# Performance work log

Hardware: AMD Instinct MI355X
Metric: run time of the kernel (lower is better)

Reference implementation:

```python
import jax, jax.numpy as jnp
import numpy as np

N = 10000      # nodes
E = 80000      # edges
D = 128        # d_model
H = 8          # num_heads
DH = 128       # d_head
DFF = 512      # d_ff
CLAMP = 5.0
EPS = 1e-5


def setup_inputs() -> dict:
    key = jax.random.key(0)
    ks = jax.random.split(key, 10)
    s = 0.05
    return {
        "feat": jax.random.normal(ks[0], (N, D), jnp.float32),
        "src": jax.random.randint(ks[1], (E,), 0, N),
        "dst": jax.random.randint(ks[2], (E,), 0, N),
        # projections stored as (in, out); x @ W == torch Linear(bias=False)
        "Wq": jax.random.normal(ks[3], (D, H * DH), jnp.float32) * s,
        "Wk": jax.random.normal(ks[4], (D, H * DH), jnp.float32) * s,
        "Wv": jax.random.normal(ks[5], (D, H * DH), jnp.float32) * s,
        "Wo": jax.random.normal(ks[6], (H * DH, D), jnp.float32) * s,
        "g1": jnp.ones((D,), jnp.float32),
        "b1": jnp.zeros((D,), jnp.float32),
        "W1": jax.random.normal(ks[7], (D, DFF), jnp.float32) * s,
        "bf1": jnp.zeros((DFF,), jnp.float32),
        "W2": jax.random.normal(ks[8], (DFF, D), jnp.float32) * s,
        "bf2": jnp.zeros((D,), jnp.float32),
        "g2": jnp.ones((D,), jnp.float32),
        "b2": jnp.zeros((D,), jnp.float32),
    }


def _layer_norm(x, g, b):
    mu = x.mean(-1, keepdims=True)
    xc = x - mu
    var = (xc * xc).mean(-1, keepdims=True)
    return xc * jax.lax.rsqrt(var + EPS) * g + b


def reference(feat, src, dst, Wq, Wk, Wv, Wo, g1, b1, W1, bf1, W2, bf2, g2, b2):
    h_src = feat[src]                              # (E, D) gather
    h_dst = feat[dst]                              # (E, D)
    q = (h_dst @ Wq).reshape(E, H, DH)             # query from destination node
    k = (h_src @ Wk).reshape(E, H, DH)
    v = (h_src @ Wv).reshape(E, H, DH)
    # per-edge logits: QK dot per head, scale, clamp
    u = jnp.clip((q * k).sum(-1) / np.sqrt(DH), -CLAMP, CLAMP)  # (E, H)
    # edge_softmax over incoming edges of each destination node
    m = jax.ops.segment_max(u, dst, num_segments=N)             # (N, H)
    ex = jnp.exp(u - m[dst])
    den = jax.ops.segment_sum(ex, dst, num_segments=N)          # (N, H)
    a = ex / den[dst]                                           # (E, H)
    # weighted V, segment-sum to destination nodes
    agg = jax.ops.segment_sum(a[..., None] * v, dst, num_segments=N)  # (N, H, DH)
    uh = _layer_norm(feat + agg.reshape(N, H * DH) @ Wo, g1, b1)
    ffn = jax.nn.relu(uh @ W1 + bf1) @ W2 + bf2
    return _layer_norm(uh + ffn, g2, b2)
```

## Files before the change

### kernel.cpp

```cpp
#include <hip/hip_runtime.h>

typedef unsigned int uint;
typedef unsigned short ushort;
typedef __attribute__((ext_vector_type(8))) short short8;
typedef __attribute__((ext_vector_type(4))) float f32x4;

#define DEV static __device__ __forceinline__

DEV float bf_lo(uint v) { return __uint_as_float(v << 16); }
DEV float bf_hi(uint v) { return __uint_as_float(v & 0xffff0000u); }
DEV ushort f2bf(float f) {
    uint u = __float_as_uint(f);
    u += 0x7fffu + ((u >> 16) & 1u);
    return (ushort)(u >> 16);
}
DEV void stC(float* p, float v) { *p = v; }
DEV void stC(ushort* p, float v) { *p = f2bf(v); }

#define DPPADD(v, ctrl) \
    ((v) + __int_as_float(__builtin_amdgcn_mov_dpp(__float_as_int(v), (ctrl), 0xF, 0xF, true)))

template <typename OT>
DEV void transp_body(float (*tile)[65], const float* __restrict__ in,
                     OT* __restrict__ out, int R, int C, int bid, int t)
{
    const int nbx = C >> 6;
    const int bx = bid % nbx, by = bid / nbx;
#pragma unroll
    for (int it = 0; it < 4; ++it) {
        int idx = it * 256 + t;
        int rr = idx >> 4, cc4 = (idx & 15) * 4;
        float4 v = *reinterpret_cast<const float4*>(in + (size_t)(by * 64 + rr) * C + bx * 64 + cc4);
        tile[cc4][rr] = v.x; tile[cc4 + 1][rr] = v.y;
        tile[cc4 + 2][rr] = v.z; tile[cc4 + 3][rr] = v.w;
    }
    __syncthreads();
#pragma unroll
    for (int it = 0; it < 4; ++it) {
        int idx = it * 256 + t;
        int cc = idx >> 4, rr4 = (idx & 15) * 4;
        OT* po = out + (size_t)(bx * 64 + cc) * R + by * 64 + rr4;
        if constexpr (__is_same(OT, float)) {
            float4 o = { tile[cc][rr4], tile[cc][rr4 + 1], tile[cc][rr4 + 2], tile[cc][rr4 + 3] };
            *reinterpret_cast<float4*>(po) = o;
        } else {
            ushort4 o = { f2bf(tile[cc][rr4]), f2bf(tile[cc][rr4 + 1]),
                          f2bf(tile[cc][rr4 + 2]), f2bf(tile[cc][rr4 + 3]) };
            *reinterpret_cast<ushort4*>(po) = o;
        }
    }
}

__global__ __launch_bounds__(256) void prep1_kernel(
    int4* __restrict__ cntd4, int nz,
    const float* __restrict__ feat, ushort* __restrict__ featbf,
    const float* __restrict__ Wo, float* __restrict__ WoT,
    const float* __restrict__ W1, ushort* __restrict__ W1T,
    const float* __restrict__ W2, ushort* __restrict__ W2T, int N)
{
    __shared__ float tile[64][65];
    const int zb = (nz + 255) / 256;
    const int nf = (N * 32 + 255) / 256;
    const int b = blockIdx.x, t = threadIdx.x;
    if (b < zb) {
        int i = b * 256 + t;
        if (i < nz) cntd4[i] = int4{0, 0, 0, 0};
    } else if (b < zb + nf) {
        int i = (b - zb) * 256 + t;
        if (i >= N * 32) return;
        float4 v = reinterpret_cast<const float4*>(feat)[i];
        ushort4 o;
        o.x = f2bf(v.x); o.y = f2bf(v.y); o.z = f2bf(v.z); o.w = f2bf(v.w);
        reinterpret_cast<ushort4*>(featbf)[i] = o;
    } else if (b < zb + nf + 32) {
        transp_body<float>(tile, Wo, WoT, 1024, 128, b - zb - nf, t);
    } else if (b < zb + nf + 48) {
        transp_body<ushort>(tile, W1, W1T, 128, 512, b - zb - nf - 32, t);
    } else {
        transp_body<ushort>(tile, W2, W2T, 512, 128, b - zb - nf - 48, t);
    }
}

__global__ __launch_bounds__(256) void hist_kernel(
    const int* __restrict__ dst, int* __restrict__ cntd, int E)
{
    int e = blockIdx.x * 256 + threadIdx.x;
    if (e >= E) return;
    atomicAdd(&cntd[dst[e]], 1);
}

__global__ __launch_bounds__(1024) void scan1_kernel(
    const int* __restrict__ cntd, int* __restrict__ offd, int* __restrict__ curd, int N)
{
    __shared__ int ls[1024];
    const int t = threadIdx.x;
    const int chunk = (N + 1023) >> 10;
    int base = t * chunk;
    int s = 0;
    for (int i = 0; i < chunk; ++i) {
        int idx = base + i;
        if (idx < N) s += cntd[idx];
    }
    ls[t] = s;
    __syncthreads();
    for (int d = 1; d < 1024; d <<= 1) {
        int v = (t >= d) ? ls[t - d] : 0;
        __syncthreads();
        ls[t] += v;
        __syncthreads();
    }
    int run = t ? ls[t - 1] : 0;
    for (int i = 0; i < chunk; ++i) {
        int idx = base + i;
        if (idx < N) {
            offd[idx] = run;
            curd[idx] = run;
            run += cntd[idx];
        }
    }
    if (t == 1023) offd[N] = run;
}

__global__ __launch_bounds__(256) void scat_mpt_kernel(
    const int* __restrict__ src, const int* __restrict__ dst,
    int* __restrict__ curd, int* __restrict__ src_d, int* __restrict__ dst_d, int E, int eb,
    const float* __restrict__ Wq, const float* __restrict__ Wk,
    const float* __restrict__ Wv, const float* __restrict__ WoT,
    ushort* __restrict__ MPT)
{
    __shared__ char lds[65536];
    const int b = blockIdx.x, t = threadIdx.x;
    if (b < eb) {
        int e = b * 256 + t;
        if (e >= E) return;
        int s = src[e], d = dst[e];
        int pd = atomicAdd(&curd[d], 1);
        src_d[pd] = s;
        dst_d[pd] = d;
        return;
    }
    char* As = lds;
    char* Bs = lds + 32768;

    const int mb = b - eb;
    const int part = mb >> 3, h = mb & 7;
    const int lane = t & 63, w = t >> 6;
    const int frow = lane & 15, kgrp = lane >> 4;

    const float* Asrc = part ? WoT : Wk;
    const float* Bsrc = part ? Wv : Wq;
    const float ascale = part ? 1.f : 0.08838834764831845f;

#pragma unroll
    for (int it = 0; it < 16; ++it) {
        int idx = it * 256 + t;
        int r = idx >> 5, c4 = (idx & 31) * 4;
        size_t goff = (size_t)r * 1024 + h * 128 + c4;
        float4 va = *reinterpret_cast<const float4*>(Asrc + goff);
        ushort4 ua = { f2bf(va.x * ascale), f2bf(va.y * ascale),
                       f2bf(va.z * ascale), f2bf(va.w * ascale) };
        *reinterpret_cast<ushort4*>(&As[r * 256 + ((c4 * 2) ^ ((r & 7) << 4))]) = ua;
        float4 vb = *reinterpret_cast<const float4*>(Bsrc + goff);
        ushort4 ub = { f2bf(vb.x), f2bf(vb.y), f2bf(vb.z), f2bf(vb.w) };
        *reinterpret_cast<ushort4*>(&Bs[r * 256 + ((c4 * 2) ^ ((r & 7) << 4))]) = ub;
    }
    __syncthreads();

    f32x4 acc[2][8] = {};
#pragma unroll
    for (int ks = 0; ks < 4; ++ks) {
        int koff = ks * 64 + kgrp * 16;
        short8 bfr[8];
#pragma unroll
        for (int fn = 0; fn < 8; ++fn) {
            int col = fn * 16 + frow;
            bfr[fn] = *reinterpret_cast<const short8*>(&Bs[col * 256 + (koff ^ ((col & 7) << 4))]);
        }
#pragma unroll
        for (int fm = 0; fm < 2; ++fm) {
            int row = w * 32 + fm * 16 + frow;
            short8 a = *reinterpret_cast<const short8*>(&As[row * 256 + (koff ^ ((row & 7) << 4))]);
#pragma unroll
            for (int fn = 0; fn < 8; ++fn)
                acc[fm][fn] = __builtin_amdgcn_mfma_f32_16x16x32_bf16(a, bfr[fn], acc[fm][fn], 0, 0, 0);
        }
    }

    const size_t base = ((size_t)part * 1024 + h * 128) * 128;
#pragma unroll
    for (int fm = 0; fm < 2; ++fm)
#pragma unroll
        for (int fn = 0; fn < 8; ++fn)
#pragma unroll
            for (int r = 0; r < 4; ++r) {
                int j = w * 32 + fm * 16 + kgrp * 4 + r;
                int i = fn * 16 + frow;
                MPT[base + (size_t)j * 128 + i] = f2bf(acc[fm][fn][r]);
            }
}

template <int NTILE, typename OT, bool BIAS, bool RELU, bool RES>
__global__ __launch_bounds__(256) void gemm_mfma(
    const ushort* __restrict__ A, const ushort* __restrict__ BT,
    const float* __restrict__ bias, const float* __restrict__ res,
    OT* __restrict__ C, int M, int K, int NC)
{
    constexpr int FN = NTILE * 2;
    constexpr int WN = NTILE * 32;
    __shared__ char lds[16384 + NTILE * 8192];
    char* AsB = lds;
    char* BsB = lds + 16384;

    const int m0 = blockIdx.y * 128;
    const int n0 = blockIdx.x * (NTILE * 64);
    const int t = threadIdx.x;
    const int lane = t & 63, wid = t >> 6;
    const int wm = wid >> 1, wn = wid & 1;
    const int frow = lane & 15, kgrp = lane >> 4;

    f32x4 acc[4][FN] = {};

    for (int kk = 0; kk < K; kk += 64) {
#pragma unroll
        for (int it = 0; it < 4; ++it) {
            int q = it * 256 + t;
            int r = q >> 3, c8 = (q & 7) * 8;
            int gm = m0 + r;
            short8 v = {};
            if (gm < M) v = *reinterpret_cast<const short8*>(&A[(size_t)gm * K + kk + c8]);
            *reinterpret_cast<short8*>(&AsB[r * 128 + ((c8 * 2) ^ ((r & 7) << 4))]) = v;
        }
#pragma unroll
        for (int it = 0; it < 2 * NTILE; ++it) {
            int q = it * 256 + t;
            int r = q >> 3, c8 = (q & 7) * 8;
            short8 v = *reinterpret_cast<const short8*>(&BT[(size_t)(n0 + r) * K + kk + c8]);
            *reinterpret_cast<short8*>(&BsB[r * 128 + ((c8 * 2) ^ ((r & 7) << 4))]) = v;
        }
        __syncthreads();
#pragma unroll
        for (int kp = 0; kp < 2; ++kp) {
            const int koffb = kp * 64 + kgrp * 16;
            short8 b[FN];
#pragma unroll
            for (int fn = 0; fn < FN; ++fn) {
                int col = wn * WN + fn * 16 + frow;
                b[fn] = *reinterpret_cast<const short8*>(&BsB[col * 128 + (koffb ^ ((col & 7) << 4))]);
            }
#pragma unroll
            for (int fm = 0; fm < 4; ++fm) {
                int row = wm * 64 + fm * 16 + frow;
                short8 a = *reinterpret_cast<const short8*>(&AsB[row * 128 + (koffb ^ ((row & 7) << 4))]);
#pragma unroll
                for (int fn = 0; fn < FN; ++fn)
                    acc[fm][fn] = __builtin_amdgcn_mfma_f32_16x16x32_bf16(a, b[fn], acc[fm][fn], 0, 0, 0);
            }
        }
        __syncthreads();
    }

#pragma unroll
    for (int fm = 0; fm < 4; ++fm)
#pragma unroll
        for (int fn = 0; fn < FN; ++fn)
#pragma unroll
            for (int r = 0; r < 4; ++r) {
                int gm = m0 + wm * 64 + fm * 16 + kgrp * 4 + r;
                int gn = n0 + wn * WN + fn * 16 + frow;
                if (gm >= M) continue;
                float v = acc[fm][fn][r];
                if (BIAS) v += bias[gn];
                if (RELU) v = fmaxf(v, 0.f);
                if (RES) v += res[(size_t)gm * NC + gn];
                stC(&C[(size_t)gm * NC + gn], v);
            }
}

__global__ __launch_bounds__(256) void gemm_mfma64(
    const ushort* __restrict__ A, const ushort* __restrict__ BT,
    const float* __restrict__ bias, const float* __restrict__ res,
    float* __restrict__ C, int M, int K, int NC)
{
    __shared__ char lds[16384];
    char* AsB = lds;
    char* BsB = lds + 8192;

    const int m0 = blockIdx.y * 64;
    const int n0 = blockIdx.x * 64;
    const int t = threadIdx.x;
    const int lane = t & 63, wid = t >> 6;
    const int wm = wid >> 1, wn = wid & 1;
    const int frow = lane & 15, kgrp = lane >> 4;

    f32x4 acc[2][2] = {};

    for (int kk = 0; kk < K; kk += 64) {
#pragma unroll
        for (int it = 0; it < 2; ++it) {
            int q = it * 256 + t;
            int r = q >> 3, c8 = (q & 7) * 8;
            int gm = m0 + r;
            short8 v = {};
            if (gm < M) v = *reinterpret_cast<const short8*>(&A[(size_t)gm * K + kk + c8]);
            *reinterpret_cast<short8*>(&AsB[r * 128 + ((c8 * 2) ^ ((r & 7) << 4))]) = v;
        }
#pragma unroll
        for (int it = 0; it < 2; ++it) {
            int q = it * 256 + t;
            int r = q >> 3, c8 = (q & 7) * 8;
            short8 v = *reinterpret_cast<const short8*>(&BT[(size_t)(n0 + r) * K + kk + c8]);
            *reinterpret_cast<short8*>(&BsB[r * 128 + ((c8 * 2) ^ ((r & 7) << 4))]) = v;
        }
        __syncthreads();
#pragma unroll
        for (int kp = 0; kp < 2; ++kp) {
            const int koffb = kp * 64 + kgrp * 16;
            short8 b[2];
#pragma unroll
            for (int fn = 0; fn < 2; ++fn) {
                int col = wn * 32 + fn * 16 + frow;
                b[fn] = *reinterpret_cast<const short8*>(&BsB[col * 128 + (koffb ^ ((col & 7) << 4))]);
            }
#pragma unroll
            for (int fm = 0; fm < 2; ++fm) {
                int row = wm * 32 + fm * 16 + frow;
                short8 a = *reinterpret_cast<const short8*>(&AsB[row * 128 + (koffb ^ ((row & 7) << 4))]);
#pragma unroll
                for (int fn = 0; fn < 2; ++fn)
                    acc[fm][fn] = __builtin_amdgcn_mfma_f32_16x16x32_bf16(a, b[fn], acc[fm][fn], 0, 0, 0);
            }
        }
        __syncthreads();
    }

#pragma unroll
    for (int fm = 0; fm < 2; ++fm)
#pragma unroll
        for (int fn = 0; fn < 2; ++fn)
#pragma unroll
            for (int r = 0; r < 4; ++r) {
                int gm = m0 + wm * 32 + fm * 16 + kgrp * 4 + r;
                int gn = n0 + wn * 32 + fn * 16 + frow;
                if (gm >= M) continue;
                float v = acc[fm][fn][r] + bias[gn] + res[(size_t)gm * NC + gn];
                C[(size_t)gm * NC + gn] = v;
            }
}

__global__ __launch_bounds__(256) void edge_logits2_kernel(
    const ushort* __restrict__ featbf, const ushort* __restrict__ GVO,
    const int* __restrict__ src_d, const int* __restrict__ dst_d,
    float* __restrict__ exws, int E)
{
    int w = (int)((blockIdx.x * 256 + threadIdx.x) >> 6);
    int lane = threadIdx.x & 63;
    int el = lane >> 4, li = lane & 15;
    int p = w * 4 + el;
    if (p >= E) return;
    int s = src_d[p], d = dst_d[p];
    uint4 f = reinterpret_cast<const uint4*>(featbf)[(size_t)s * 16 + li];
    const uint4* Grow = reinterpret_cast<const uint4*>(GVO) + (size_t)d * 256 + li;
    float sel = 0.f;
#pragma unroll
    for (int h = 0; h < 8; ++h) {
        uint4 g = Grow[h * 16];
        float pv = bf_lo(g.x) * bf_lo(f.x) + bf_hi(g.x) * bf_hi(f.x);
        pv += bf_lo(g.y) * bf_lo(f.y) + bf_hi(g.y) * bf_hi(f.y);
        pv += bf_lo(g.z) * bf_lo(f.z) + bf_hi(g.z) * bf_hi(f.z);
        pv += bf_lo(g.w) * bf_lo(f.w) + bf_hi(g.w) * bf_hi(f.w);
        pv = DPPADD(pv, 0xB1);
        pv = DPPADD(pv, 0x4E);
        pv = DPPADD(pv, 0x141);
        pv = DPPADD(pv, 0x128);
        sel = (li == h) ? pv : sel;
    }
    float u = fminf(fmaxf(sel, -5.f), 5.f);
    float ex = __expf(u);
    if (li < 8) exws[(size_t)p * 8 + li] = ex;
}

__global__ __launch_bounds__(256) void aggden_ln1_kernel(
    const ushort* __restrict__ GVO, const int* __restrict__ src_d,
    const int* __restrict__ offd, const float* __restrict__ exws,
    const float* __restrict__ feat, const float* __restrict__ g1,
    const float* __restrict__ b1, float* __restrict__ uh,
    ushort* __restrict__ uhbf, int N)
{
    int d = (int)((blockIdx.x * 256 + threadIdx.x) >> 6);
    int lane = threadIdx.x & 63;
    if (d >= N) return;
    const int lo = offd[d], hi = offd[d + 1];

    int h = lane & 7;
    float den = 0.f;
    for (int i = lo + (lane >> 3); i < hi; i += 8)
        den += exws[(size_t)i * 8 + h];
    den += __shfl_xor(den, 8);
    den += __shfl_xor(den, 16);
    den += __shfl_xor(den, 32);
    float rh = 1.f / den;
    float rv0 = __shfl(rh, 0), rv1 = __shfl(rh, 1), rv2 = __shfl(rh, 2), rv3 = __shfl(rh, 3);
    float rv4 = __shfl(rh, 4), rv5 = __shfl(rh, 5), rv6 = __shfl(rh, 6), rv7 = __shfl(rh, 7);

    float acc0 = 0.f, acc1 = 0.f;
    int snext = (lo < hi) ? src_d[lo] : 0;
    for (int i = lo; i < hi; ++i) {
        int s = snext;
        if (i + 1 < hi) snext = src_d[i + 1];
        float4 e0 = *reinterpret_cast<const float4*>(&exws[(size_t)i * 8]);
        float4 e1 = *reinterpret_cast<const float4*>(&exws[(size_t)i * 8 + 4]);
        const uint* vrow = reinterpret_cast<const uint*>(GVO + (size_t)s * 2048 + 1024);
        uint gv0 = vrow[0 * 64 + lane], gv1 = vrow[1 * 64 + lane];
        uint gv2 = vrow[2 * 64 + lane], gv3 = vrow[3 * 64 + lane];
        uint gv4 = vrow[4 * 64 + lane], gv5 = vrow[5 * 64 + lane];
        uint gv6 = vrow[6 * 64 + lane], gv7 = vrow[7 * 64 + lane];
        float a0 = e0.x * rv0, a1 = e0.y * rv1, a2 = e0.z * rv2, a3 = e0.w * rv3;
        float a4 = e1.x * rv4, a5 = e1.y * rv5, a6 = e1.z * rv6, a7 = e1.w * rv7;
        acc0 += a0 * bf_lo(gv0) + a1 * bf_lo(gv1) + a2 * bf_lo(gv2) + a3 * bf_lo(gv3)
              + a4 * bf_lo(gv4) + a5 * bf_lo(gv5) + a6 * bf_lo(gv6) + a7 * bf_lo(gv7);
        acc1 += a0 * bf_hi(gv0) + a1 * bf_hi(gv1) + a2 * bf_hi(gv2) + a3 * bf_hi(gv3)
              + a4 * bf_hi(gv4) + a5 * bf_hi(gv5) + a6 * bf_hi(gv6) + a7 * bf_hi(gv7);
    }

    float2 v = reinterpret_cast<const float2*>(feat)[(size_t)d * 64 + lane];
    v.x += acc0;
    v.y += acc1;
    float sum = v.x + v.y;
#pragma unroll
    for (int off = 32; off; off >>= 1) sum += __shfl_xor(sum, off);
    float mean = sum * (1.f / 128.f);
    float cx = v.x - mean, cy = v.y - mean;
    float vs = cx * cx + cy * cy;
#pragma unroll
    for (int off = 32; off; off >>= 1) vs += __shfl_xor(vs, off);
    float r = rsqrtf(vs * (1.f / 128.f) + 1e-5f);
    float2 gg = reinterpret_cast<const float2*>(g1)[lane];
    float2 bb = reinterpret_cast<const float2*>(b1)[lane];
    float2 o;
    o.x = cx * r * gg.x + bb.x;
    o.y = cy * r * gg.y + bb.y;
    reinterpret_cast<float2*>(uh)[(size_t)d * 64 + lane] = o;
    ushort2 ob; ob.x = f2bf(o.x); ob.y = f2bf(o.y);
    reinterpret_cast<ushort2*>(uhbf)[(size_t)d * 64 + lane] = ob;
}

__global__ __launch_bounds__(256) void ln_kernel(
    const float* __restrict__ x, const float* __restrict__ g,
    const float* __restrict__ b, float* __restrict__ out, int M)
{
    int row = (int)((blockIdx.x * 256 + threadIdx.x) >> 6);
    int lane = threadIdx.x & 63;
    if (row >= M) return;
    float2 v = reinterpret_cast<const float2*>(x)[(size_t)row * 64 + lane];
    float sum = v.x + v.y;
#pragma unroll
    for (int off = 32; off; off >>= 1) sum += __shfl_xor(sum, off);
    float mean = sum * (1.f / 128.f);
    float cx = v.x - mean, cy = v.y - mean;
    float vs = cx * cx + cy * cy;
#pragma unroll
    for (int off = 32; off; off >>= 1) vs += __shfl_xor(vs, off);
    float r = rsqrtf(vs * (1.f / 128.f) + 1e-5f);
    float2 gg = reinterpret_cast<const float2*>(g)[lane];
    float2 bb = reinterpret_cast<const float2*>(b)[lane];
    float2 o;
    o.x = cx * r * gg.x + bb.x;
    o.y = cy * r * gg.y + bb.y;
    reinterpret_cast<float2*>(out)[(size_t)row * 64 + lane] = o;
}

extern "C" void kernel_launch(void* const* d_in, const int* in_sizes, int n_in,
                              void* d_out, int out_size, void* d_ws, size_t ws_size,
                              hipStream_t stream)
{
    const float* feat = (const float*)d_in[0];
    const int*   src  = (const int*)d_in[1];
    const int*   dst  = (const int*)d_in[2];
    const float* Wq   = (const float*)d_in[3];
    const float* Wk   = (const float*)d_in[4];
    const float* Wv   = (const float*)d_in[5];
    const float* Wo   = (const float*)d_in[6];
    const float* g1   = (const float*)d_in[7];
    const float* b1   = (const float*)d_in[8];
    const float* W1   = (const float*)d_in[9];
    const float* bf1  = (const float*)d_in[10];
    const float* W2   = (const float*)d_in[11];
    const float* bf2  = (const float*)d_in[12];
    const float* g2   = (const float*)d_in[13];
    const float* b2   = (const float*)d_in[14];
    const int N = in_sizes[0] / 128;
    const int E = in_sizes[1];
    float* out = (float*)d_out;

    char* w = (char*)d_ws;
    auto alloc = [&](size_t bytes) {
        char* p = w;
        w += (bytes + 255) & ~(size_t)255;
        return p;
    };
    ushort* MPT    = (ushort*)alloc((size_t)2048 * 128 * 2);
    float*  WoT    = (float*)alloc((size_t)128 * 1024 * 4);
    ushort* W1T    = (ushort*)alloc((size_t)512 * 128 * 2);
    ushort* W2T    = (ushort*)alloc((size_t)128 * 512 * 2);
    ushort* featbf = (ushort*)alloc((size_t)N * 128 * 2);
    ushort* GVO    = (ushort*)alloc((size_t)N * 2048 * 2);
    float*  exws   = (float*)alloc((size_t)E * 8 * 4);
    int*    cntd   = (int*)alloc((size_t)((N + 3) & ~3) * 4);
    int*    offd   = (int*)alloc((size_t)(N + 1) * 4);
    int*    curd   = (int*)alloc((size_t)N * 4);
    int*    src_d  = (int*)alloc((size_t)E * 4);
    int*    dst_d  = (int*)alloc((size_t)E * 4);
    float*  uh     = (float*)alloc((size_t)N * 128 * 4);
    ushort* uhbf   = (ushort*)alloc((size_t)N * 128 * 2);
    ushort* f1     = (ushort*)alloc((size_t)N * 512 * 2);
    float*  pre2   = (float*)alloc((size_t)N * 128 * 4);

    int nz = (N + 3) / 4;
    int zb = (nz + 255) / 256;
    int nf = (N * 32 + 255) / 256;
    prep1_kernel<<<zb + nf + 64, 256, 0, stream>>>(
        (int4*)cntd, nz, feat, featbf, Wo, WoT, W1, W1T, W2, W2T, N);

    int eb = (E + 255) / 256;
    hist_kernel<<<eb, 256, 0, stream>>>(dst, cntd, E);
    scan1_kernel<<<1, 1024, 0, stream>>>(cntd, offd, curd, N);
    scat_mpt_kernel<<<eb + 16, 256, 0, stream>>>(
        src, dst, curd, src_d, dst_d, E, eb, Wq, Wk, Wv, WoT, MPT);

    dim3 gv_grid(2048 / 128, (N + 127) / 128);
    gemm_mfma<2, ushort, false, false, false><<<gv_grid, 256, 0, stream>>>(
        featbf, MPT, nullptr, nullptr, GVO, N, 128, 2048);

    edge_logits2_kernel<<<(E + 15) / 16, 256, 0, stream>>>(featbf, GVO, src_d, dst_d, exws, E);
    int nwaves_n = (N * 64 + 255) / 256;
    aggden_ln1_kernel<<<nwaves_n, 256, 0, stream>>>(
        GVO, src_d, offd, exws, feat, g1, b1, uh, uhbf, N);

    dim3 f1_grid(512 / 128, (N + 127) / 128);
    gemm_mfma<2, ushort, true, true, false><<<f1_grid, 256, 0, stream>>>(
        uhbf, W1T, bf1, nullptr, f1, N, 128, 512);
    dim3 f2_grid(128 / 64, (N + 63) / 64);
    gemm_mfma64<<<f2_grid, 256, 0, stream>>>(
        f1, W2T, bf2, uh, pre2, N, 512, 128);

    ln_kernel<<<nwaves_n, 256, 0, stream>>>(pre2, g2, b2, out, N);
}
```

Baseline: 127.6 us.

## Regroup launches: fuse histogram with MPT, scan with GVO GEMM, edge logits with aggregation

Restructures the graph-preprocessing and edge stages to cut kernel launches and overlap independent work. The destination histogram now runs in the same launch as the weight-product (MPT) blocks. The prefix scan becomes one extra block inside the GVO GEMM launch, and the edge scatter gets its own small kernel. Edge-logit computation is fused into the per-node aggregation/LN1 kernel, with each block handling four destination nodes and their contiguous CSR edge range. The trade-offs are a 256-thread scan replacing the 1024-thread one, uneven per-block work from degree skew, and an extra block barrier in the fused kernel.

```diff
diff --git a/kernel.cpp b/kernel.cpp
--- a/kernel.cpp
+++ b/kernel.cpp
@@ -81,49 +81,8 @@
     }
 }
 
-__global__ __launch_bounds__(256) void hist_kernel(
-    const int* __restrict__ dst, int* __restrict__ cntd, int E)
-{
-    int e = blockIdx.x * 256 + threadIdx.x;
-    if (e >= E) return;
-    atomicAdd(&cntd[dst[e]], 1);
-}
-
-__global__ __launch_bounds__(1024) void scan1_kernel(
-    const int* __restrict__ cntd, int* __restrict__ offd, int* __restrict__ curd, int N)
-{
-    __shared__ int ls[1024];
-    const int t = threadIdx.x;
-    const int chunk = (N + 1023) >> 10;
-    int base = t * chunk;
-    int s = 0;
-    for (int i = 0; i < chunk; ++i) {
-        int idx = base + i;
-        if (idx < N) s += cntd[idx];
-    }
-    ls[t] = s;
-    __syncthreads();
-    for (int d = 1; d < 1024; d <<= 1) {
-        int v = (t >= d) ? ls[t - d] : 0;
-        __syncthreads();
-        ls[t] += v;
-        __syncthreads();
-    }
-    int run = t ? ls[t - 1] : 0;
-    for (int i = 0; i < chunk; ++i) {
-        int idx = base + i;
-        if (idx < N) {
-            offd[idx] = run;
-            curd[idx] = run;
-            run += cntd[idx];
-        }
-    }
-    if (t == 1023) offd[N] = run;
-}
-
-__global__ __launch_bounds__(256) void scat_mpt_kernel(
-    const int* __restrict__ src, const int* __restrict__ dst,
-    int* __restrict__ curd, int* __restrict__ src_d, int* __restrict__ dst_d, int E, int eb,
+__global__ __launch_bounds__(256) void hist_mpt_kernel(
+    const int* __restrict__ dst, int* __restrict__ cntd, int E, int eb,
     const float* __restrict__ Wq, const float* __restrict__ Wk,
     const float* __restrict__ Wv, const float* __restrict__ WoT,
     ushort* __restrict__ MPT)
@@ -132,11 +91,7 @@
     const int b = blockIdx.x, t = threadIdx.x;
     if (b < eb) {
         int e = b * 256 + t;
-        if (e >= E) return;
-        int s = src[e], d = dst[e];
-        int pd = atomicAdd(&curd[d], 1);
-        src_d[pd] = s;
-        dst_d[pd] = d;
+        if (e < E) atomicAdd(&cntd[dst[e]], 1);
         return;
     }
     char* As = lds;
@@ -199,61 +154,89 @@
             }
 }
 
-template <int NTILE, typename OT, bool BIAS, bool RELU, bool RES>
-__global__ __launch_bounds__(256) void gemm_mfma(
+__global__ __launch_bounds__(256) void scan_gvo_kernel(
+    const int* __restrict__ cntd, int* __restrict__ offd, int* __restrict__ curd, int N,
     const ushort* __restrict__ A, const ushort* __restrict__ BT,
-    const float* __restrict__ bias, const float* __restrict__ res,
-    OT* __restrict__ C, int M, int K, int NC)
-{
-    constexpr int FN = NTILE * 2;
-    constexpr int WN = NTILE * 32;
-    __shared__ char lds[16384 + NTILE * 8192];
+    ushort* __restrict__ C, int nbg)
+{
+    __shared__ char lds[32768];
+    const int b = blockIdx.x, t = threadIdx.x;
+
+    if (b >= nbg) {
+        int* ls = (int*)lds;
+        const int chunk = (N + 255) >> 8;
+        int base = t * chunk;
+        int s = 0;
+        for (int i = 0; i < chunk; ++i) {
+            int idx = base + i;
+            if (idx < N) s += cntd[idx];
+        }
+        ls[t] = s;
+        __syncthreads();
+        for (int d = 1; d < 256; d <<= 1) {
+            int v = (t >= d) ? ls[t - d] : 0;
+            __syncthreads();
+            ls[t] += v;
+            __syncthreads();
+        }
+        int run = t ? ls[t - 1] : 0;
+        for (int i = 0; i < chunk; ++i) {
+            int idx = base + i;
+            if (idx < N) {
+                offd[idx] = run;
+                curd[idx] = run;
+                run += cntd[idx];
+            }
+        }
+        if (t == 255) offd[N] = run;
+        return;
+    }
+
     char* AsB = lds;
     char* BsB = lds + 16384;
-
-    const int m0 = blockIdx.y * 128;
-    const int n0 = blockIdx.x * (NTILE * 64);
-    const int t = threadIdx.x;
+    const int M = N;
+    const int m0 = (b >> 4) * 128;
+    const int n0 = (b & 15) * 128;
     const int lane = t & 63, wid = t >> 6;
     const int wm = wid >> 1, wn = wid & 1;
     const int frow = lane & 15, kgrp = lane >> 4;
 
-    f32x4 acc[4][FN] = {};
-
-    for (int kk = 0; kk < K; kk += 64) {
+    f32x4 acc[4][4] = {};
+
+    for (int kk = 0; kk < 128; kk += 64) {
 #pragma unroll
         for (int it = 0; it < 4; ++it) {
             int q = it * 256 + t;
             int r = q >> 3, c8 = (q & 7) * 8;
             int gm = m0 + r;
             short8 v = {};
-            if (gm < M) v = *reinterpret_cast<const short8*>(&A[(size_t)gm * K + kk + c8]);
+            if (gm < M) v = *reinterpret_cast<const short8*>(&A[(size_t)gm * 128 + kk + c8]);
             *reinterpret_cast<short8*>(&AsB[r * 128 + ((c8 * 2) ^ ((r & 7) << 4))]) = v;
         }
 #pragma unroll
-        for (int it = 0; it < 2 * NTILE; ++it) {
+        for (int it = 0; it < 4; ++it) {
             int q = it * 256 + t;
             int r = q >> 3, c8 = (q & 7) * 8;
-            short8 v = *reinterpret_cast<const short8*>(&BT[(size_t)(n0 + r) * K + kk + c8]);
+            short8 v = *reinterpret_cast<const short8*>(&BT[(size_t)(n0 + r) * 128 + kk + c8]);
             *reinterpret_cast<short8*>(&BsB[r * 128 + ((c8 * 2) ^ ((r & 7) << 4))]) = v;
         }
         __syncthreads();
 #pragma unroll
         for (int kp = 0; kp < 2; ++kp) {
             const int koffb = kp * 64 + kgrp * 16;
-            short8 b[FN];
-#pragma unroll
-            for (int fn = 0; fn < FN; ++fn) {
-                int col = wn * WN + fn * 16 + frow;
-                b[fn] = *reinterpret_cast<const short8*>(&BsB[col * 128 + (koffb ^ ((col & 7) << 4))]);
+            short8 bb[4];
+#pragma unroll
+            for (int fn = 0; fn < 4; ++fn) {
+                int col = wn * 64 + fn * 16 + frow;
+                bb[fn] = *reinterpret_cast<const short8*>(&BsB[col * 128 + (koffb ^ ((col & 7) << 4))]);
             }
 #pragma unroll
             for (int fm = 0; fm < 4; ++fm) {
                 int row = wm * 64 + fm * 16 + frow;
                 short8 a = *reinterpret_cast<const short8*>(&AsB[row * 128 + (koffb ^ ((row & 7) << 4))]);
 #pragma unroll
-                for (int fn = 0; fn < FN; ++fn)
-                    acc[fm][fn] = __builtin_amdgcn_mfma_f32_16x16x32_bf16(a, b[fn], acc[fm][fn], 0, 0, 0);
+                for (int fn = 0; fn < 4; ++fn)
+                    acc[fm][fn] = __builtin_amdgcn_mfma_f32_16x16x32_bf16(a, bb[fn], acc[fm][fn], 0, 0, 0);
             }
         }
         __syncthreads();
@@ -262,132 +245,71 @@
 #pragma unroll
     for (int fm = 0; fm < 4; ++fm)
 #pragma unroll
-        for (int fn = 0; fn < FN; ++fn)
+        for (int fn = 0; fn < 4; ++fn)
 #pragma unroll
             for (int r = 0; r < 4; ++r) {
                 int gm = m0 + wm * 64 + fm * 16 + kgrp * 4 + r;
-                int gn = n0 + wn * WN + fn * 16 + frow;
+                int gn = n0 + wn * 64 + fn * 16 + frow;
                 if (gm >= M) continue;
-                float v = acc[fm][fn][r];
-                if (BIAS) v += bias[gn];
-                if (RELU) v = fmaxf(v, 0.f);
-                if (RES) v += res[(size_t)gm * NC + gn];
-                stC(&C[(size_t)gm * NC + gn], v);
-            }
-}
-
-__global__ __launch_bounds__(256) void gemm_mfma64(
-    const ushort* __restrict__ A, const ushort* __restrict__ BT,
-    const float* __restrict__ bias, const float* __restrict__ res,
-    float* __restrict__ C, int M, int K, int NC)
-{
-    __shared__ char lds[16384];
-    char* AsB = lds;
-    char* BsB = lds + 8192;
-
-    const int m0 = blockIdx.y * 64;
-    const int n0 = blockIdx.x * 64;
-    const int t = threadIdx.x;
-    const int lane = t & 63, wid = t >> 6;
-    const int wm = wid >> 1, wn = wid & 1;
-    const int frow = lane & 15, kgrp = lane >> 4;
-
-    f32x4 acc[2][2] = {};
-
-    for (int kk = 0; kk < K; kk += 64) {
-#pragma unroll
-        for (int it = 0; it < 2; ++it) {
-            int q = it * 256 + t;
-            int r = q >> 3, c8 = (q & 7) * 8;
-            int gm = m0 + r;
-            short8 v = {};
-            if (gm < M) v = *reinterpret_cast<const short8*>(&A[(size_t)gm * K + kk + c8]);
-            *reinterpret_cast<short8*>(&AsB[r * 128 + ((c8 * 2) ^ ((r & 7) << 4))]) = v;
-        }
-#pragma unroll
-        for (int it = 0; it < 2; ++it) {
-            int q = it * 256 + t;
-            int r = q >> 3, c8 = (q & 7) * 8;
-            short8 v = *reinterpret_cast<const short8*>(&BT[(size_t)(n0 + r) * K + kk + c8]);
-            *reinterpret_cast<short8*>(&BsB[r * 128 + ((c8 * 2) ^ ((r & 7) << 4))]) = v;
-        }
-        __syncthreads();
-#pragma unroll
-        for (int kp = 0; kp < 2; ++kp) {
-            const int koffb = kp * 64 + kgrp * 16;
-            short8 b[2];
-#pragma unroll
-            for (int fn = 0; fn < 2; ++fn) {
-                int col = wn * 32 + fn * 16 + frow;
-                b[fn] = *reinterpret_cast<const short8*>(&BsB[col * 128 + (koffb ^ ((col & 7) << 4))]);
-            }
-#pragma unroll
-            for (int fm = 0; fm < 2; ++fm) {
-                int row = wm * 32 + fm * 16 + frow;
-                short8 a = *reinterpret_cast<const short8*>(&AsB[row * 128 + (koffb ^ ((row & 7) << 4))]);
-#pragma unroll
-                for (int fn = 0; fn < 2; ++fn)
-                    acc[fm][fn] = __builtin_amdgcn_mfma_f32_16x16x32_bf16(a, b[fn], acc[fm][fn], 0, 0, 0);
-            }
-        }
-        __syncthreads();
-    }
-
-#pragma unroll
-    for (int fm = 0; fm < 2; ++fm)
-#pragma unroll
-        for (int fn = 0; fn < 2; ++fn)
-#pragma unroll
-            for (int r = 0; r < 4; ++r) {
-                int gm = m0 + wm * 32 + fm * 16 + kgrp * 4 + r;
-                int gn = n0 + wn * 32 + fn * 16 + frow;
-                if (gm >= M) continue;
-                float v = acc[fm][fn][r] + bias[gn] + res[(size_t)gm * NC + gn];
-                C[(size_t)gm * NC + gn] = v;
-            }
-}
-
-__global__ __launch_bounds__(256) void edge_logits2_kernel(
+                stC(&C[(size_t)gm * 2048 + gn], acc[fm][fn][r]);
+            }
+}
+
+__global__ void scat_kernel(const int* __restrict__ src, const int* __restrict__ dst,
+                            int* __restrict__ curd,
+                            int* __restrict__ src_d, int* __restrict__ dst_d, int E)
+{
+    int e = blockIdx.x * 256 + threadIdx.x;
+    if (e >= E) return;
+    int s = src[e], d = dst[e];
+    int pd = atomicAdd(&curd[d], 1);
+    src_d[pd] = s;
+    dst_d[pd] = d;
+}
+
+__global__ __launch_bounds__(256) void edge_fused_kernel(
     const ushort* __restrict__ featbf, const ushort* __restrict__ GVO,
     const int* __restrict__ src_d, const int* __restrict__ dst_d,
-    float* __restrict__ exws, int E)
-{
-    int w = (int)((blockIdx.x * 256 + threadIdx.x) >> 6);
-    int lane = threadIdx.x & 63;
-    int el = lane >> 4, li = lane & 15;
-    int p = w * 4 + el;
-    if (p >= E) return;
-    int s = src_d[p], d = dst_d[p];
-    uint4 f = reinterpret_cast<const uint4*>(featbf)[(size_t)s * 16 + li];
-    const uint4* Grow = reinterpret_cast<const uint4*>(GVO) + (size_t)d * 256 + li;
-    float sel = 0.f;
-#pragma unroll
-    for (int h = 0; h < 8; ++h) {
-        uint4 g = Grow[h * 16];
-        float pv = bf_lo(g.x) * bf_lo(f.x) + bf_hi(g.x) * bf_hi(f.x);
-        pv += bf_lo(g.y) * bf_lo(f.y) + bf_hi(g.y) * bf_hi(f.y);
-        pv += bf_lo(g.z) * bf_lo(f.z) + bf_hi(g.z) * bf_hi(f.z);
-        pv += bf_lo(g.w) * bf_lo(f.w) + bf_hi(g.w) * bf_hi(f.w);
-        pv = DPPADD(pv, 0xB1);
-        pv = DPPADD(pv, 0x4E);
-        pv = DPPADD(pv, 0x141);
-        pv = DPPADD(pv, 0x128);
-        sel = (li == h) ? pv : sel;
-    }
-    float u = fminf(fmaxf(sel, -5.f), 5.f);
-    float ex = __expf(u);
-    if (li < 8) exws[(size_t)p * 8 + li] = ex;
-}
-
-__global__ __launch_bounds__(256) void aggden_ln1_kernel(
-    const ushort* __restrict__ GVO, const int* __restrict__ src_d,
-    const int* __restrict__ offd, const float* __restrict__ exws,
+    const int* __restrict__ offd, float* __restrict__ exws,
     const float* __restrict__ feat, const float* __restrict__ g1,
     const float* __restrict__ b1, float* __restrict__ uh,
     ushort* __restrict__ uhbf, int N)
 {
-    int d = (int)((blockIdx.x * 256 + threadIdx.x) >> 6);
-    int lane = threadIdx.x & 63;
+    const int d0 = blockIdx.x * 4;
+    const int t = threadIdx.x;
+    const int blo = offd[d0];
+    const int bhi = offd[min(d0 + 4, N)];
+
+    {
+        int g = t >> 4, li = t & 15;
+        for (int p = blo + g; p < bhi; p += 16) {
+            int s = src_d[p], d = dst_d[p];
+            uint4 f = reinterpret_cast<const uint4*>(featbf)[(size_t)s * 16 + li];
+            const uint4* Grow = reinterpret_cast<const uint4*>(GVO) + (size_t)d * 256 + li;
+            float sel = 0.f;
+#pragma unroll
+            for (int h = 0; h < 8; ++h) {
+                uint4 gv = Grow[h * 16];
+                float pv = bf_lo(gv.x) * bf_lo(f.x) + bf_hi(gv.x) * bf_hi(f.x);
+                pv += bf_lo(gv.y) * bf_lo(f.y) + bf_hi(gv.y) * bf_hi(f.y);
+                pv += bf_lo(gv.z) * bf_lo(f.z) + bf_hi(gv.z) * bf_hi(f.z);
+                pv += bf_lo(gv.w) * bf_lo(f.w) + bf_hi(gv.w) * bf_hi(f.w);
+                pv = DPPADD(pv, 0xB1);
+                pv = DPPADD(pv, 0x4E);
+                pv = DPPADD(pv, 0x141);
+                pv = DPPADD(pv, 0x128);
+                sel = (li == h) ? pv : sel;
+            }
+            float u = fminf(fmaxf(sel, -5.f), 5.f);
+            float ex = __expf(u);
+            if (li < 8) exws[(size_t)p * 8 + li] = ex;
+        }
+    }
+    __threadfence_block();
+    __syncthreads();
+
+    const int lane = t & 63;
+    const int d = d0 + (t >> 6);
     if (d >= N) return;
     const int lo = offd[d], hi = offd[d + 1];
 
@@ -442,6 +364,154 @@
     reinterpret_cast<float2*>(uh)[(size_t)d * 64 + lane] = o;
     ushort2 ob; ob.x = f2bf(o.x); ob.y = f2bf(o.y);
     reinterpret_cast<ushort2*>(uhbf)[(size_t)d * 64 + lane] = ob;
+}
+
+template <int NTILE, typename OT, bool BIAS, bool RELU, bool RES>
+__global__ __launch_bounds__(256) void gemm_mfma(
+    const ushort* __restrict__ A, const ushort* __restrict__ BT,
+    const float* __restrict__ bias, const float* __restrict__ res,
+    OT* __restrict__ C, int M, int K, int NC)
+{
+    constexpr int FN = NTILE * 2;
+    constexpr int WN = NTILE * 32;
+    __shared__ char lds[16384 + NTILE * 8192];
+    char* AsB = lds;
+    char* BsB = lds + 16384;
+
+    const int m0 = blockIdx.y * 128;
+    const int n0 = blockIdx.x * (NTILE * 64);
+    const int t = threadIdx.x;
+    const int lane = t & 63, wid = t >> 6;
+    const int wm = wid >> 1, wn = wid & 1;
+    const int frow = lane & 15, kgrp = lane >> 4;
+
+    f32x4 acc[4][FN] = {};
+
+    for (int kk = 0; kk < K; kk += 64) {
+#pragma unroll
+        for (int it = 0; it < 4; ++it) {
+            int q = it * 256 + t;
+            int r = q >> 3, c8 = (q & 7) * 8;
+            int gm = m0 + r;
+            short8 v = {};
+            if (gm < M) v = *reinterpret_cast<const short8*>(&A[(size_t)gm * K + kk + c8]);
+            *reinterpret_cast<short8*>(&AsB[r * 128 + ((c8 * 2) ^ ((r & 7) << 4))]) = v;
+        }
+#pragma unroll
+        for (int it = 0; it < 2 * NTILE; ++it) {
+            int q = it * 256 + t;
+            int r = q >> 3, c8 = (q & 7) * 8;
+            short8 v = *reinterpret_cast<const short8*>(&BT[(size_t)(n0 + r) * K + kk + c8]);
+            *reinterpret_cast<short8*>(&BsB[r * 128 + ((c8 * 2) ^ ((r & 7) << 4))]) = v;
+        }
+        __syncthreads();
+#pragma unroll
+        for (int kp = 0; kp < 2; ++kp) {
+            const int koffb = kp * 64 + kgrp * 16;
+            short8 b[FN];
+#pragma unroll
+            for (int fn = 0; fn < FN; ++fn) {
+                int col = wn * WN + fn * 16 + frow;
+                b[fn] = *reinterpret_cast<const short8*>(&BsB[col * 128 + (koffb ^ ((col & 7) << 4))]);
+            }
+#pragma unroll
+            for (int fm = 0; fm < 4; ++fm) {
+                int row = wm * 64 + fm * 16 + frow;
+                short8 a = *reinterpret_cast<const short8*>(&AsB[row * 128 + (koffb ^ ((row & 7) << 4))]);
+#pragma unroll
+                for (int fn = 0; fn < FN; ++fn)
+                    acc[fm][fn] = __builtin_amdgcn_mfma_f32_16x16x32_bf16(a, b[fn], acc[fm][fn], 0, 0, 0);
+            }
+        }
+        __syncthreads();
+    }
+
+#pragma unroll
+    for (int fm = 0; fm < 4; ++fm)
+#pragma unroll
+        for (int fn = 0; fn < FN; ++fn)
+#pragma unroll
+            for (int r = 0; r < 4; ++r) {
+                int gm = m0 + wm * 64 + fm * 16 + kgrp * 4 + r;
+                int gn = n0 + wn * WN + fn * 16 + frow;
+                if (gm >= M) continue;
+                float v = acc[fm][fn][r];
+                if (BIAS) v += bias[gn];
+                if (RELU) v = fmaxf(v, 0.f);
+                if (RES) v += res[(size_t)gm * NC + gn];
+                stC(&C[(size_t)gm * NC + gn], v);
+            }
+}
+
+__global__ __launch_bounds__(256) void gemm_mfma64(
+    const ushort* __restrict__ A, const ushort* __restrict__ BT,
+    const float* __restrict__ bias, const float* __restrict__ res,
+    float* __restrict__ C, int M, int K, int NC)
+{
+    __shared__ char lds[16384];
+    char* AsB = lds;
+    char* BsB = lds + 8192;
+
+    const int m0 = blockIdx.y * 64;
+    const int n0 = blockIdx.x * 64;
+    const int t = threadIdx.x;
+    const int lane = t & 63, wid = t >> 6;
+    const int wm = wid >> 1, wn = wid & 1;
+    const int frow = lane & 15, kgrp = lane >> 4;
+
+    f32x4 acc[2][2] = {};
+
+    for (int kk = 0; kk < K; kk += 64) {
+#pragma unroll
+        for (int it = 0; it < 2; ++it) {
+            int q = it * 256 + t;
+            int r = q >> 3, c8 = (q & 7) * 8;
+            int gm = m0 + r;
+            short8 v = {};
+            if (gm < M) v = *reinterpret_cast<const short8*>(&A[(size_t)gm * K + kk + c8]);
+            *reinterpret_cast<short8*>(&AsB[r * 128 + ((c8 * 2) ^ ((r & 7) << 4))]) = v;
+        }
+#pragma unroll
+        for (int it = 0; it < 2; ++it) {
+            int q = it * 256 + t;
+            int r = q >> 3, c8 = (q & 7) * 8;
+            short8 v = *reinterpret_cast<const short8*>(&BT[(size_t)(n0 + r) * K + kk + c8]);
+            *reinterpret_cast<short8*>(&BsB[r * 128 + ((c8 * 2) ^ ((r & 7) << 4))]) = v;
+        }
+        __syncthreads();
+#pragma unroll
+        for (int kp = 0; kp < 2; ++kp) {
+            const int koffb = kp * 64 + kgrp * 16;
+            short8 b[2];
+#pragma unroll
+            for (int fn = 0; fn < 2; ++fn) {
+                int col = wn * 32 + fn * 16 + frow;
+                b[fn] = *reinterpret_cast<const short8*>(&BsB[col * 128 + (koffb ^ ((col & 7) << 4))]);
+            }
+#pragma unroll
+            for (int fm = 0; fm < 2; ++fm) {
+                int row = wm * 32 + fm * 16 + frow;
+                short8 a = *reinterpret_cast<const short8*>(&AsB[row * 128 + (koffb ^ ((row & 7) << 4))]);
+#pragma unroll
+                for (int fn = 0; fn < 2; ++fn)
+                    acc[fm][fn] = __builtin_amdgcn_mfma_f32_16x16x32_bf16(a, b[fn], acc[fm][fn], 0, 0, 0);
+            }
+        }
+        __syncthreads();
+    }
+
+#pragma unroll
+    for (int fm = 0; fm < 2; ++fm)
+#pragma unroll
+        for (int fn = 0; fn < 2; ++fn)
+#pragma unroll
+            for (int r = 0; r < 4; ++r) {
+                int gm = m0 + wm * 32 + fm * 16 + kgrp * 4 + r;
+                int gn = n0 + wn * 32 + fn * 16 + frow;
+                if (gm >= M) continue;
+                float v = acc[fm][fn][r] + bias[gn] + res[(size_t)gm * NC + gn];
+                C[(size_t)gm * NC + gn] = v;
+            }
 }
 
 __global__ __launch_bounds__(256) void ln_kernel(
@@ -522,19 +592,17 @@
         (int4*)cntd, nz, feat, featbf, Wo, WoT, W1, W1T, W2, W2T, N);
 
     int eb = (E + 255) / 256;
-    hist_kernel<<<eb, 256, 0, stream>>>(dst, cntd, E);
-    scan1_kernel<<<1, 1024, 0, stream>>>(cntd, offd, curd, N);
-    scat_mpt_kernel<<<eb + 16, 256, 0, stream>>>(
-        src, dst, curd, src_d, dst_d, E, eb, Wq, Wk, Wv, WoT, MPT);
-
-    dim3 gv_grid(2048 / 128, (N + 127) / 128);
-    gemm_mfma<2, ushort, false, false, false><<<gv_grid, 256, 0, stream>>>(
-        featbf, MPT, nullptr, nullptr, GVO, N, 128, 2048);
-
-    edge_logits2_kernel<<<(E + 15) / 16, 256, 0, stream>>>(featbf, GVO, src_d, dst_d, exws, E);
-    int nwaves_n = (N * 64 + 255) / 256;
-    aggden_ln1_kernel<<<nwaves_n, 256, 0, stream>>>(
-        GVO, src_d, offd, exws, feat, g1, b1, uh, uhbf, N);
+    hist_mpt_kernel<<<eb + 16, 256, 0, stream>>>(
+        dst, cntd, E, eb, Wq, Wk, Wv, WoT, MPT);
+
+    int nbg = 16 * ((N + 127) / 128);
+    scan_gvo_kernel<<<nbg + 1, 256, 0, stream>>>(
+        cntd, offd, curd, N, featbf, MPT, GVO, nbg);
+
+    scat_kernel<<<eb, 256, 0, stream>>>(src, dst, curd, src_d, dst_d, E);
+
+    edge_fused_kernel<<<(N + 3) / 4, 256, 0, stream>>>(
+        featbf, GVO, src_d, dst_d, offd, exws, feat, g1, b1, uh, uhbf, N);
 
     dim3 f1_grid(512 / 128, (N + 127) / 128);
     gemm_mfma<2, ushort, true, true, false><<<f1_grid, 256, 0, stream>>>(
@@ -542,6 +610,6 @@
     dim3 f2_grid(128 / 64, (N + 63) / 64);
     gemm_mfma64<<<f2_grid, 256, 0, stream>>>(
         f1, W2T, bf2, uh, pre2, N, 512, 128);
-
+    int nwaves_n = (N * 64 + 255) / 256;
     ln_kernel<<<nwaves_n, 256, 0, stream>>>(pre2, g2, b2, out, N);
 }
```

After: 135.0 us. 1.06x slower.
